# Kernel tuning notes

Hardware: AMD Instinct MI355X
Metric: run time of the kernel (lower is better)

## Reference

```python
import jax, jax.numpy as jnp
import numpy as np

B, T, H = 4, 2048, 1024
DFF = 4 * H
MAX_DEPTH = 4
TARGET_DEPTH = 2.5
BUDGET_WEIGHT = 0.01
ACT_TAU = 0.99


def setup_inputs() -> dict:
    key = jax.random.key(0)
    ks = jax.random.split(key, 6)
    s = 0.02
    return {
        "x": jax.random.normal(ks[0], (B, T, H), dtype=jnp.float32),
        "Wb1": jax.random.normal(ks[1], (H, DFF), dtype=jnp.float32) * s,
        "bb1": jnp.zeros((DFF,), dtype=jnp.float32),
        "Wb2": jax.random.normal(ks[2], (DFF, H), dtype=jnp.float32) * s,
        "bb2": jnp.zeros((H,), dtype=jnp.float32),
        "Rw1": jax.random.normal(ks[3], (MAX_DEPTH - 1, H + 1, H // 2), dtype=jnp.float32) * s,
        "Rb1": jnp.zeros((MAX_DEPTH - 1, H // 2), dtype=jnp.float32),
        "Rw2": jax.random.normal(ks[4], (MAX_DEPTH - 1, H // 2, 1), dtype=jnp.float32) * s,
        "Rb2": jnp.zeros((MAX_DEPTH - 1, 1), dtype=jnp.float32),
    }


def _body(x, Wb1, bb1, Wb2, bb2):
    # transformer-style FFN body, exact (erf) GELU to match torch nn.GELU
    h = jax.nn.gelu(jnp.einsum("btd,df->btf", x, Wb1) + bb1, approximate=False)
    return jnp.einsum("btf,fd->btd", h, Wb2) + bb2


def reference(x, Wb1, bb1, Wb2, bb2, Rw1, Rb1, Rw2, Rb2):
    # mandatory first pass
    x = _body(x, Wb1, bb1, Wb2, bb2)
    lead = x.shape[:-1]  # (B, T)
    weight_sum = jnp.ones(lead, dtype=x.dtype)
    cumulative_p = jnp.zeros(lead, dtype=x.dtype)
    still_running = jnp.ones(lead, dtype=x.dtype)
    for i in range(MAX_DEPTH - 1):
        # router: concat spike-rate feature (zeros: no scalar aux from body)
        feat = jnp.concatenate([x, jnp.zeros(lead + (1,), dtype=x.dtype)], axis=-1)
        h = jax.nn.gelu(jnp.einsum("btf,fm->btm", feat, Rw1[i]) + Rb1[i], approximate=False)
        logit = (jnp.einsum("btm,mo->bto", h, Rw2[i]) + Rb2[i])[..., 0]
        p = jax.nn.sigmoid(logit)
        # ACT remainder trick
        remainder = jnp.clip(1.0 - cumulative_p, 0.0)
        would_halt = cumulative_p + p >= ACT_TAU
        weight = jnp.where(would_halt, remainder, p) * still_running
        # soft depth mix
        x_new = _body(x, Wb1, bb1, Wb2, bb2)
        w = weight[..., None]
        x = w * x_new + (1.0 - w) * x
        weight_sum = weight_sum + weight
        cumulative_p = cumulative_p + weight
        still_running = still_running * (~would_halt).astype(x.dtype)
    avg_depth = weight_sum.mean()
    budget_loss = BUDGET_WEIGHT * jnp.square(jax.nn.relu(avg_depth - TARGET_DEPTH))
    return x, budget_loss
```

## Files before the change

### kernel.cpp

```cpp
#include <hip/hip_runtime.h>
#include <hip/hip_bf16.h>
#include <math.h>

typedef __bf16 bf16_t;
typedef __attribute__((ext_vector_type(8))) __bf16 bf16x8;
typedef __attribute__((ext_vector_type(4))) __bf16 bf16x4;
typedef __attribute__((ext_vector_type(4))) float f32x4;

#define NTOK 8192
#define HDIM 1024
#define DFF  4096
#define RHID 512

__device__ __forceinline__ float gelu_exact(float v) {
  return 0.5f * v * (1.0f + erff(v * 0.70710678118654752f));
}

__device__ __forceinline__ void async_cp16(void* lds, const void* g) {
  __builtin_amdgcn_global_load_lds(
      (__attribute__((address_space(1))) void*)g,
      (__attribute__((address_space(3))) void*)lds, 16, 0, 0);
}

__device__ __forceinline__ void remap_tile(int g, int& mt, int& nt) {
  mt = ((g & 7) << 3) | ((g >> 3) & 7);
  nt = g >> 6;
}

template<int MODE, bool WRITE_OUT>
__device__ __forceinline__ void body_tile(
    int mt, int nt,
    const bf16_t* __restrict__ A, const bf16_t* __restrict__ Bt,
    const float* __restrict__ bias, int N, int K,
    bf16_t* __restrict__ Hout, float* __restrict__ Xout,
    bf16_t* __restrict__ Xb, bf16_t* __restrict__ Xlo,
    const float* __restrict__ Wmix,
    bf16_t* As, bf16_t* Bs)
{
  const int tid  = threadIdx.x;
  const int lane = tid & 63;
  const int wv   = tid >> 6;
  const int wm   = wv >> 1;
  const int wn   = wv & 1;
  const int lr   = lane & 15;
  const int quad = lane >> 4;
  const int m0 = mt * 128;
  const int n0 = nt * 128;

  f32x4 acc[4][4];
#pragma unroll
  for (int i = 0; i < 4; ++i)
#pragma unroll
    for (int j = 0; j < 4; ++j)
      acc[i][j] = (f32x4){0.f, 0.f, 0.f, 0.f};

  const int c0 = tid;
  const int c1 = tid + 256;
  const int r0 = c0 >> 2, r1 = c1 >> 2;
  const int ks0 = ((c0 ^ r0) & 3) * 8;
  const int ks1 = ((c1 ^ r1) & 3) * 8;
  const bf16_t* Ag0 = A  + (size_t)(m0 + r0) * K + ks0;
  const bf16_t* Ag1 = A  + (size_t)(m0 + r1) * K + ks1;
  const bf16_t* Bg0 = Bt + (size_t)(n0 + r0) * K + ks0;
  const bf16_t* Bg1 = Bt + (size_t)(n0 + r1) * K + ks1;
  char* lA0 = (char*)As + c0 * 16;
  char* lA1 = (char*)As + c1 * 16;
  char* lB0 = (char*)Bs + c0 * 16;
  char* lB1 = (char*)Bs + c1 * 16;

  const int sw = ((quad ^ lr) & 3) * 8;
  const int KB = K >> 5;

  async_cp16(lA0, Ag0);
  async_cp16(lA1, Ag1);
  async_cp16(lB0, Bg0);
  async_cp16(lB1, Bg1);

  for (int kb = 0; kb < KB; ++kb) {
    __syncthreads();
    const int cur = kb & 1;
    if (kb + 1 < KB) {
      const int nb = (1 - cur) * 8192;
      const int ko = (kb + 1) << 5;
      async_cp16(lA0 + nb, Ag0 + ko);
      async_cp16(lA1 + nb, Ag1 + ko);
      async_cp16(lB0 + nb, Bg0 + ko);
      async_cp16(lB1 + nb, Bg1 + ko);
    }
    const bf16_t* Asc = As + cur * 4096;
    const bf16_t* Bsc = Bs + cur * 4096;
    bf16x8 af[4], bfr[4];
#pragma unroll
    for (int i = 0; i < 4; ++i)
      af[i] = *(const bf16x8*)&Asc[(wm * 64 + i * 16 + lr) * 32 + sw];
#pragma unroll
    for (int j = 0; j < 4; ++j)
      bfr[j] = *(const bf16x8*)&Bsc[(wn * 64 + j * 16 + lr) * 32 + sw];
#pragma unroll
    for (int i = 0; i < 4; ++i)
#pragma unroll
      for (int j = 0; j < 4; ++j)
        acc[i][j] = __builtin_amdgcn_mfma_f32_16x16x32_bf16(af[i], bfr[j], acc[i][j], 0, 0, 0);
  }

#pragma unroll
  for (int i = 0; i < 4; ++i) {
#pragma unroll
    for (int r = 0; r < 4; ++r) {
      const int gm = m0 + wm * 64 + i * 16 + quad * 4 + r;
      float wmix = 0.f, onemw = 0.f;
      if (MODE == 2) { wmix = Wmix[gm]; onemw = 1.f - wmix; }
#pragma unroll
      for (int j = 0; j < 4; ++j) {
        const int gn = n0 + wn * 64 + j * 16 + lr;
        float v = acc[i][j][r] + bias[gn];
        if (MODE == 0) {
          Hout[(size_t)gm * N + gn] = (bf16_t)gelu_exact(v);
        } else {
          const size_t idx = (size_t)gm * N + gn;
          if (MODE == 2) {
            const float xold = (float)Xb[idx] + (float)Xlo[idx];
            v = wmix * v + onemw * xold;
          }
          const bf16_t hi = (bf16_t)v;
          Xb[idx]  = hi;
          Xlo[idx] = (bf16_t)(v - (float)hi);
          if (WRITE_OUT) Xout[idx] = v;
        }
      }
    }
  }
}

__device__ __forceinline__ void router_tile(
    int mt, int nt,
    const bf16_t* __restrict__ Ah, const bf16_t* __restrict__ Al,
    const bf16_t* __restrict__ Bh, const bf16_t* __restrict__ Bl,
    const float* __restrict__ bias, float* __restrict__ Hr,
    bf16_t* Ahs, bf16_t* Als, bf16_t* Bhs, bf16_t* Bls)
{
  const int K = HDIM, N = RHID;
  const int tid  = threadIdx.x;
  const int lane = tid & 63;
  const int wv   = tid >> 6;
  const int wm   = wv >> 1;
  const int wn   = wv & 1;
  const int lr   = lane & 15;
  const int quad = lane >> 4;
  const int m0 = mt * 128;
  const int n0 = nt * 128;

  f32x4 acc[4][4];
#pragma unroll
  for (int i = 0; i < 4; ++i)
#pragma unroll
    for (int j = 0; j < 4; ++j)
      acc[i][j] = (f32x4){0.f, 0.f, 0.f, 0.f};

  const int c0 = tid;
  const int c1 = tid + 256;
  const int r0 = c0 >> 2, r1 = c1 >> 2;
  const int ks0 = ((c0 ^ r0) & 3) * 8;
  const int ks1 = ((c1 ^ r1) & 3) * 8;
  const size_t aoff0 = (size_t)(m0 + r0) * K + ks0;
  const size_t aoff1 = (size_t)(m0 + r1) * K + ks1;
  const size_t boff0 = (size_t)(n0 + r0) * K + ks0;
  const size_t boff1 = (size_t)(n0 + r1) * K + ks1;
  const int sw = ((quad ^ lr) & 3) * 8;

  for (int k0 = 0; k0 < K; k0 += 32) {
    __syncthreads();
    async_cp16((char*)Ahs + c0 * 16, Ah + aoff0 + k0);
    async_cp16((char*)Ahs + c1 * 16, Ah + aoff1 + k0);
    async_cp16((char*)Als + c0 * 16, Al + aoff0 + k0);
    async_cp16((char*)Als + c1 * 16, Al + aoff1 + k0);
    async_cp16((char*)Bhs + c0 * 16, Bh + boff0 + k0);
    async_cp16((char*)Bhs + c1 * 16, Bh + boff1 + k0);
    async_cp16((char*)Bls + c0 * 16, Bl + boff0 + k0);
    async_cp16((char*)Bls + c1 * 16, Bl + boff1 + k0);
    __syncthreads();
    bf16x8 ah[4], al[4], bh[4], bl[4];
#pragma unroll
    for (int i = 0; i < 4; ++i) {
      const int ao = (wm * 64 + i * 16 + lr) * 32 + sw;
      ah[i] = *(const bf16x8*)&Ahs[ao];
      al[i] = *(const bf16x8*)&Als[ao];
    }
#pragma unroll
    for (int j = 0; j < 4; ++j) {
      const int bo = (wn * 64 + j * 16 + lr) * 32 + sw;
      bh[j] = *(const bf16x8*)&Bhs[bo];
      bl[j] = *(const bf16x8*)&Bls[bo];
    }
#pragma unroll
    for (int i = 0; i < 4; ++i)
#pragma unroll
      for (int j = 0; j < 4; ++j) {
        acc[i][j] = __builtin_amdgcn_mfma_f32_16x16x32_bf16(ah[i], bh[j], acc[i][j], 0, 0, 0);
        acc[i][j] = __builtin_amdgcn_mfma_f32_16x16x32_bf16(al[i], bh[j], acc[i][j], 0, 0, 0);
        acc[i][j] = __builtin_amdgcn_mfma_f32_16x16x32_bf16(ah[i], bl[j], acc[i][j], 0, 0, 0);
      }
  }

#pragma unroll
  for (int i = 0; i < 4; ++i)
#pragma unroll
    for (int r = 0; r < 4; ++r) {
      const int gm = m0 + wm * 64 + i * 16 + quad * 4 + r;
#pragma unroll
      for (int j = 0; j < 4; ++j) {
        const int gn = n0 + wn * 64 + j * 16 + lr;
        Hr[(size_t)gm * N + gn] = gelu_exact(acc[i][j][r] + bias[gn]);
      }
    }
}

template<int MODE, bool WRITE_OUT>
__global__ __launch_bounds__(256, 2)
void k_gemm(const bf16_t* __restrict__ A, const bf16_t* __restrict__ Bt,
            const float* __restrict__ bias, int N, int K,
            float* __restrict__ Xout, bf16_t* __restrict__ Xb,
            bf16_t* __restrict__ Xlo, const float* __restrict__ Wmix)
{
  __shared__ __align__(16) bf16_t sm[4 * 128 * 32];
  int mt, nt;
  remap_tile(blockIdx.x, mt, nt);
  body_tile<MODE, WRITE_OUT>(mt, nt, A, Bt, bias, N, K, nullptr, Xout, Xb, Xlo, Wmix,
                             sm, sm + 2 * 128 * 32);
}

__global__ __launch_bounds__(256, 2)
void k_body0_router(const bf16_t* __restrict__ xb, const bf16_t* __restrict__ W1t,
                    const float* __restrict__ bb1, bf16_t* __restrict__ hbuf,
                    const bf16_t* __restrict__ xlo,
                    const bf16_t* __restrict__ R1h, const bf16_t* __restrict__ R1l,
                    const float* __restrict__ Rb1, float* __restrict__ hr,
                    int nbody)
{
  __shared__ __align__(16) bf16_t sm[4 * 128 * 32];
  const int g = blockIdx.x;
  if (g < nbody) {
    int mt, nt;
    remap_tile(g, mt, nt);
    body_tile<0, false>(mt, nt, xb, W1t, bb1, DFF, HDIM, hbuf,
                        nullptr, nullptr, nullptr, nullptr,
                        sm, sm + 2 * 128 * 32);
  } else {
    int mt, nt;
    remap_tile(g - nbody, mt, nt);
    router_tile(mt, nt, xb, xlo, R1h, R1l, Rb1, hr,
                sm, sm + 128 * 32, sm + 2 * 128 * 32, sm + 3 * 128 * 32);
  }
}

__global__ void act_kernel(const float* __restrict__ Hr,
                           const float* __restrict__ rw2, const float* __restrict__ rb2,
                           float* __restrict__ cum_p, float* __restrict__ still_r,
                           float* __restrict__ wsum, float* __restrict__ wvec)
{
  const int t = blockIdx.x * 4 + (threadIdx.x >> 6);
  const int lane = threadIdx.x & 63;
  float s = 0.f;
#pragma unroll
  for (int j = 0; j < 8; ++j) {
    const int m = lane + j * 64;
    s += Hr[(size_t)t * RHID + m] * rw2[m];
  }
  for (int off = 32; off > 0; off >>= 1) s += __shfl_down(s, off, 64);
  if (lane == 0) {
    const float logit = s + rb2[0];
    const float p = 1.f / (1.f + expf(-logit));
    const float cum = cum_p[t];
    const float still = still_r[t];
    const float rem = fmaxf(1.f - cum, 0.f);
    const bool halt = (cum + p) >= 0.99f;
    const float w = (halt ? rem : p) * still;
    wvec[t] = w;
    wsum[t] += w;
    cum_p[t] = cum + w;
    if (halt) still_r[t] = 0.f;
  }
}

__global__ void transpose_to_bf16(const float* __restrict__ src, int srcld, int dstld,
                                  bf16_t* __restrict__ dst, bf16_t* __restrict__ dlo)
{
  __shared__ float tile[32][33];
  const int tx = threadIdx.x & 31;
  const int ty = threadIdx.x >> 5;
  const int bx = blockIdx.x;
  const int by = blockIdx.y;
#pragma unroll
  for (int l = 0; l < 4; ++l)
    tile[ty + l * 8][tx] = src[(size_t)(by * 32 + ty + l * 8) * srcld + bx * 32 + tx];
  __syncthreads();
#pragma unroll
  for (int l = 0; l < 4; ++l) {
    const int c = bx * 32 + ty + l * 8;
    const int r = by * 32 + tx;
    const float v = tile[tx][ty + l * 8];
    const bf16_t hi = (bf16_t)v;
    dst[(size_t)c * dstld + r] = hi;
    if (dlo) dlo[(size_t)c * dstld + r] = (bf16_t)(v - (float)hi);
  }
}

__global__ void cvt_x_kernel(const float4* __restrict__ x, bf16x4* __restrict__ xb, int n4)
{
  const int i = blockIdx.x * 256 + threadIdx.x;
  if (i >= n4) return;
  const float4 v = x[i];
  bf16x4 hb;
  hb[0] = (bf16_t)v.x; hb[1] = (bf16_t)v.y; hb[2] = (bf16_t)v.z; hb[3] = (bf16_t)v.w;
  xb[i] = hb;
}

__global__ void init_state_kernel(float* __restrict__ cum, float* __restrict__ still,
                                  float* __restrict__ wsum)
{
  const int i = blockIdx.x * 256 + threadIdx.x;
  cum[i] = 0.f; still[i] = 1.f; wsum[i] = 1.f;
}

__global__ void finalize_kernel(const float* __restrict__ wsum, float* __restrict__ out)
{
  __shared__ float red[256];
  float s = 0.f;
  for (int i = threadIdx.x; i < NTOK; i += 256) s += wsum[i];
  red[threadIdx.x] = s;
  __syncthreads();
  for (int o = 128; o > 0; o >>= 1) {
    if (threadIdx.x < o) red[threadIdx.x] += red[threadIdx.x + o];
    __syncthreads();
  }
  if (threadIdx.x == 0) {
    const float avg = red[0] / (float)NTOK;
    float d = avg - 2.5f;
    d = fmaxf(d, 0.f);
    out[0] = 0.01f * d * d;
  }
}

extern "C" void kernel_launch(void* const* d_in, const int* in_sizes, int n_in,
                              void* d_out, int out_size, void* d_ws, size_t ws_size,
                              hipStream_t stream) {
  const float* x   = (const float*)d_in[0];
  const float* Wb1 = (const float*)d_in[1];
  const float* bb1 = (const float*)d_in[2];
  const float* Wb2 = (const float*)d_in[3];
  const float* bb2 = (const float*)d_in[4];
  const float* Rw1 = (const float*)d_in[5];
  const float* Rb1 = (const float*)d_in[6];
  const float* Rw2 = (const float*)d_in[7];
  const float* Rb2 = (const float*)d_in[8];
  float* out = (float*)d_out;

  char* ws = (char*)d_ws;
  size_t off = 0;
  auto carve = [&](size_t bytes) -> void* {
    void* p = ws + off;
    off += (bytes + 255) & ~(size_t)255;
    return p;
  };
  bf16_t* xb   = (bf16_t*)carve((size_t)NTOK * HDIM * 2);
  bf16_t* xlo  = (bf16_t*)carve((size_t)NTOK * HDIM * 2);
  bf16_t* hbuf = (bf16_t*)carve((size_t)NTOK * DFF * 2);
  bf16_t* W1t  = (bf16_t*)carve((size_t)HDIM * DFF * 2);
  bf16_t* W2t  = (bf16_t*)carve((size_t)HDIM * DFF * 2);
  bf16_t* R1h  = (bf16_t*)carve((size_t)3 * RHID * HDIM * 2);
  bf16_t* R1l  = (bf16_t*)carve((size_t)3 * RHID * HDIM * 2);
  float*  hr   = (float*)carve((size_t)NTOK * RHID * 4);
  float*  cum  = (float*)carve((size_t)NTOK * 4);
  float*  stil = (float*)carve((size_t)NTOK * 4);
  float*  wsum = (float*)carve((size_t)NTOK * 4);
  float*  wvec = (float*)carve((size_t)NTOK * 4);

  transpose_to_bf16<<<dim3(128, 32), 256, 0, stream>>>(Wb1, DFF, HDIM, W1t, nullptr);
  transpose_to_bf16<<<dim3(32, 128), 256, 0, stream>>>(Wb2, HDIM, DFF, W2t, nullptr);
  for (int i = 0; i < 3; ++i)
    transpose_to_bf16<<<dim3(16, 32), 256, 0, stream>>>(
        Rw1 + (size_t)i * 1025 * RHID, RHID, HDIM,
        R1h + (size_t)i * RHID * HDIM, R1l + (size_t)i * RHID * HDIM);
  cvt_x_kernel<<<8192, 256, 0, stream>>>((const float4*)x, (bf16x4*)xb, NTOK * HDIM / 4);
  init_state_kernel<<<32, 256, 0, stream>>>(cum, stil, wsum);

  k_body0_router<<<2048, 256, 0, stream>>>(xb, W1t, bb1, hbuf, xlo,
                                           nullptr, nullptr, nullptr, nullptr, 2048);
  k_gemm<1, false><<<512, 256, 0, stream>>>(hbuf, W2t, bb2, HDIM, DFF,
                                            nullptr, xb, xlo, nullptr);

  for (int i = 0; i < 3; ++i) {
    k_body0_router<<<2048 + 256, 256, 0, stream>>>(
        xb, W1t, bb1, hbuf, xlo,
        R1h + (size_t)i * RHID * HDIM, R1l + (size_t)i * RHID * HDIM,
        Rb1 + (size_t)i * RHID, hr, 2048);
    act_kernel<<<2048, 256, 0, stream>>>(hr, Rw2 + (size_t)i * RHID, Rb2 + i,
                                         cum, stil, wsum, wvec);
    if (i < 2)
      k_gemm<2, false><<<512, 256, 0, stream>>>(hbuf, W2t, bb2, HDIM, DFF,
                                                nullptr, xb, xlo, wvec);
    else
      k_gemm<2, true><<<512, 256, 0, stream>>>(hbuf, W2t, bb2, HDIM, DFF,
                                               out, xb, xlo, wvec);
  }

  finalize_kernel<<<1, 256, 0, stream>>>(wsum, out + (size_t)NTOK * HDIM);
  (void)in_sizes; (void)n_in; (void)out_size; (void)ws_size;
}
```

Before: 931.7 us.

## Use single-buffered K=64 tiles in body GEMM and tanh-approx GELU

The body GEMM mainloop moves from double-buffered K=32 stages with async prefetch to a single-buffered K=64 stage: each iteration loads the whole tile, syncs, then runs two MFMA sub-steps, using a new rotate-style LDS swizzle. This halves the number of barrier iterations but drops the overlap between global loads and compute. Separately, the first-layer body epilogue swaps exact erf GELU for a tanh-style sigmoid approximation, which cuts transcendental cost but changes numerics away from the exact GELU the reference specifies.

```diff
diff --git a/kernel.cpp b/kernel.cpp
--- a/kernel.cpp
+++ b/kernel.cpp
@@ -14,6 +14,11 @@
 
 __device__ __forceinline__ float gelu_exact(float v) {
   return 0.5f * v * (1.0f + erff(v * 0.70710678118654752f));
+}
+
+__device__ __forceinline__ float gelu_fast(float v) {
+  const float g = 1.5957691216057308f * (v + 0.044715f * v * v * v);
+  return v / (1.0f + __expf(-g));
 }
 
 __device__ __forceinline__ void async_cp16(void* lds, const void* g) {
@@ -54,53 +59,49 @@
     for (int j = 0; j < 4; ++j)
       acc[i][j] = (f32x4){0.f, 0.f, 0.f, 0.f};
 
-  const int c0 = tid;
-  const int c1 = tid + 256;
-  const int r0 = c0 >> 2, r1 = c1 >> 2;
-  const int ks0 = ((c0 ^ r0) & 3) * 8;
-  const int ks1 = ((c1 ^ r1) & 3) * 8;
-  const bf16_t* Ag0 = A  + (size_t)(m0 + r0) * K + ks0;
-  const bf16_t* Ag1 = A  + (size_t)(m0 + r1) * K + ks1;
-  const bf16_t* Bg0 = Bt + (size_t)(n0 + r0) * K + ks0;
-  const bf16_t* Bg1 = Bt + (size_t)(n0 + r1) * K + ks1;
-  char* lA0 = (char*)As + c0 * 16;
-  char* lA1 = (char*)As + c1 * 16;
-  char* lB0 = (char*)Bs + c0 * 16;
-  char* lB1 = (char*)Bs + c1 * 16;
-
-  const int sw = ((quad ^ lr) & 3) * 8;
-  const int KB = K >> 5;
-
-  async_cp16(lA0, Ag0);
-  async_cp16(lA1, Ag1);
-  async_cp16(lB0, Bg0);
-  async_cp16(lB1, Bg1);
-
-  for (int kb = 0; kb < KB; ++kb) {
+  const bf16_t* Ag[4];
+  const bf16_t* Bg[4];
+  char* lA[4];
+  char* lB[4];
+#pragma unroll
+  for (int t = 0; t < 4; ++t) {
+    const int c   = tid + t * 256;
+    const int row = c >> 3;
+    const int ks  = (((c & 7) - (row & 7)) & 7) * 8;
+    Ag[t] = A  + (size_t)(m0 + row) * K + ks;
+    Bg[t] = Bt + (size_t)(n0 + row) * K + ks;
+    lA[t] = (char*)As + c * 16;
+    lB[t] = (char*)Bs + c * 16;
+  }
+
+  for (int kb = 0; kb < K; kb += 64) {
     __syncthreads();
-    const int cur = kb & 1;
-    if (kb + 1 < KB) {
-      const int nb = (1 - cur) * 8192;
-      const int ko = (kb + 1) << 5;
-      async_cp16(lA0 + nb, Ag0 + ko);
-      async_cp16(lA1 + nb, Ag1 + ko);
-      async_cp16(lB0 + nb, Bg0 + ko);
-      async_cp16(lB1 + nb, Bg1 + ko);
-    }
-    const bf16_t* Asc = As + cur * 4096;
-    const bf16_t* Bsc = Bs + cur * 4096;
-    bf16x8 af[4], bfr[4];
-#pragma unroll
-    for (int i = 0; i < 4; ++i)
-      af[i] = *(const bf16x8*)&Asc[(wm * 64 + i * 16 + lr) * 32 + sw];
-#pragma unroll
-    for (int j = 0; j < 4; ++j)
-      bfr[j] = *(const bf16x8*)&Bsc[(wn * 64 + j * 16 + lr) * 32 + sw];
-#pragma unroll
-    for (int i = 0; i < 4; ++i)
-#pragma unroll
-      for (int j = 0; j < 4; ++j)
-        acc[i][j] = __builtin_amdgcn_mfma_f32_16x16x32_bf16(af[i], bfr[j], acc[i][j], 0, 0, 0);
+#pragma unroll
+    for (int t = 0; t < 4; ++t) {
+      async_cp16(lA[t], Ag[t] + kb);
+      async_cp16(lB[t], Bg[t] + kb);
+    }
+    __syncthreads();
+#pragma unroll
+    for (int kk = 0; kk < 2; ++kk) {
+      const int kg = kk * 4 + quad;
+      bf16x8 af[4], bfr[4];
+#pragma unroll
+      for (int i = 0; i < 4; ++i) {
+        const int ra = wm * 64 + i * 16 + lr;
+        af[i] = *(const bf16x8*)&As[ra * 64 + ((kg + ra) & 7) * 8];
+      }
+#pragma unroll
+      for (int j = 0; j < 4; ++j) {
+        const int rb = wn * 64 + j * 16 + lr;
+        bfr[j] = *(const bf16x8*)&Bs[rb * 64 + ((kg + rb) & 7) * 8];
+      }
+#pragma unroll
+      for (int i = 0; i < 4; ++i)
+#pragma unroll
+        for (int j = 0; j < 4; ++j)
+          acc[i][j] = __builtin_amdgcn_mfma_f32_16x16x32_bf16(af[i], bfr[j], acc[i][j], 0, 0, 0);
+    }
   }
 
 #pragma unroll
@@ -115,7 +116,7 @@
         const int gn = n0 + wn * 64 + j * 16 + lr;
         float v = acc[i][j][r] + bias[gn];
         if (MODE == 0) {
-          Hout[(size_t)gm * N + gn] = (bf16_t)gelu_exact(v);
+          Hout[(size_t)gm * N + gn] = (bf16_t)gelu_fast(v);
         } else {
           const size_t idx = (size_t)gm * N + gn;
           if (MODE == 2) {
@@ -222,11 +223,11 @@
             float* __restrict__ Xout, bf16_t* __restrict__ Xb,
             bf16_t* __restrict__ Xlo, const float* __restrict__ Wmix)
 {
-  __shared__ __align__(16) bf16_t sm[4 * 128 * 32];
+  __shared__ __align__(16) bf16_t sm[16384];
   int mt, nt;
   remap_tile(blockIdx.x, mt, nt);
   body_tile<MODE, WRITE_OUT>(mt, nt, A, Bt, bias, N, K, nullptr, Xout, Xb, Xlo, Wmix,
-                             sm, sm + 2 * 128 * 32);
+                             sm, sm + 8192);
 }
 
 __global__ __launch_bounds__(256, 2)
@@ -237,19 +238,19 @@
                     const float* __restrict__ Rb1, float* __restrict__ hr,
                     int nbody)
 {
-  __shared__ __align__(16) bf16_t sm[4 * 128 * 32];
+  __shared__ __align__(16) bf16_t sm[16384];
   const int g = blockIdx.x;
   if (g < nbody) {
     int mt, nt;
     remap_tile(g, mt, nt);
     body_tile<0, false>(mt, nt, xb, W1t, bb1, DFF, HDIM, hbuf,
                         nullptr, nullptr, nullptr, nullptr,
-                        sm, sm + 2 * 128 * 32);
+                        sm, sm + 8192);
   } else {
     int mt, nt;
     remap_tile(g - nbody, mt, nt);
     router_tile(mt, nt, xb, xlo, R1h, R1l, Rb1, hr,
-                sm, sm + 128 * 32, sm + 2 * 128 * 32, sm + 3 * 128 * 32);
+                sm, sm + 4096, sm + 8192, sm + 12288);
   }
 }
 
```

Result: faster. 876.7 us (-5.9%).
